# Kernel tuning notes

Measured on AMD Instinct MI355X. Metric: run time of the kernel, lower is better.

The kernel has to match this reference:

```python
import jax, jax.numpy as jnp
import numpy as np
from jax import lax

W_WIN = 7  # window size from init_kwargs


def _dwconv(x, k):
    """Depthwise 2D conv, SAME padding, kernel k: [C,1,kh,kw] (OIHW)."""
    C = x.shape[1]
    p = k.shape[-1] // 2
    return lax.conv_general_dilated(
        x, k, window_strides=(1, 1), padding=[(p, p), (p, p)],
        feature_group_count=C, dimension_numbers=("NCHW", "OIHW", "NCHW"))


def setup_inputs() -> dict:
    key = jax.random.key(0)
    ks = jax.random.split(key, 6)
    B, C, H, Wd = 1, 48, 56, 56
    x = jax.random.normal(ks[0], (B, C, H, Wd), dtype=jnp.float32)
    # small init scale keeps the softmax logits (dot/49) in a sane range
    w3 = jax.random.normal(ks[1], (C, 1, 3, 3), dtype=jnp.float32) * 0.1
    w5 = jax.random.normal(ks[2], (C, 1, 5, 5), dtype=jnp.float32) * 0.1
    w7 = jax.random.normal(ks[3], (C, 1, 7, 7), dtype=jnp.float32) * 0.1
    pw = jax.random.normal(ks[4], (C, 3 * C, 1, 1), dtype=jnp.float32) * 0.05
    pb = jax.random.normal(ks[5], (C,), dtype=jnp.float32) * 0.01
    return {"x": x, "w3": w3, "w5": w5, "w7": w7, "pw": pw, "pb": pb}


def reference(x, w3, w5, w7, pw, pb):
    B, C, H, Wd = x.shape
    w = W_WIN
    # multi-scale depthwise branch, concat on channels -> [B, 3C, H, W]
    y = jnp.concatenate([_dwconv(x, w3), _dwconv(x, w5), _dwconv(x, w7)], axis=1)
    pad_h = (-H) % w
    pad_w = (-Wd) % w
    if pad_h or pad_w:  # static Python ints -> jit-safe
        y = jnp.pad(y, ((0, 0), (0, 0), (0, pad_h), (0, pad_w)), mode="reflect")
    Hp, Wp = y.shape[2], y.shape[3]
    nH, nW = Hp // w, Wp // w
    C3 = 3 * C
    # equivalent to torch unfold(2,w,w).unfold(3,w,w).permute(0,1,2,4,3,5)
    # .reshape(B,3C,nH*nW,w*w): same row-major linearization
    yw = y.reshape(B, C3, nH * nW, w * w)
    # rows: (B, nH*nW, 3C) flattened -> N x (w*w)
    yf = yw.transpose(0, 2, 1, 3).reshape(B * nH * nW * C3, w * w)
    # full N x N self-attention over all rows (faithful to the original)
    attn = jax.nn.softmax((yf @ yf.T) / (w * w), axis=-1)
    y_hat = (attn @ yf).reshape(B, nH, nW, C3, w, w)
    y_hat = y_hat.transpose(0, 3, 1, 4, 2, 5).reshape(B, C3, nH * w, nW * w)
    y_hat = y_hat[:, :, :H, :Wd]
    # 1x1 projection 3C -> C, plus residual
    out = jnp.einsum("oi,bihw->bohw", pw[:, :, 0, 0], y_hat) + pb[None, :, None, None]
    return x + out
```

## Files before the change

kernel.cpp:

```cpp
#include <hip/hip_runtime.h>

typedef unsigned int uint;
typedef unsigned short ushort;
typedef __attribute__((ext_vector_type(8))) short bf16x8;
typedef __attribute__((ext_vector_type(4))) float f32x4;

#define C_IN   48
#define C3     144
#define HW     56
#define SSP    3136
#define DW     49
#define DPAD   64
#define NROWS  9216

#define NSPLIT 12
#define TPS    12

#define CSC 0.02944245f

#define YF_B    0
#define YFT_B   1179648
#define OPART_B 2359296
#define ESUM_B  (OPART_B + NSPLIT * DW * NROWS * 2)


__device__ __forceinline__ ushort f32_to_bf16_rne(float x) {
  uint b = __float_as_uint(x);
  b += 0x7fffu + ((b >> 16) & 1u);
  return (ushort)(b >> 16);
}
__device__ __forceinline__ float bf16_to_f32(ushort u) {
  return __uint_as_float(((uint)u) << 16);
}
__device__ __forceinline__ void async_copy16(const void* g, void* l) {
  __builtin_amdgcn_global_load_lds(
      (const __attribute__((address_space(1))) unsigned int*)g,
      (__attribute__((address_space(3))) unsigned int*)l, 16, 0, 0);
}

__global__ __launch_bounds__(256) void conv_kernel(
    const float* __restrict__ x, const float* __restrict__ w3,
    const float* __restrict__ w5, const float* __restrict__ w7,
    ushort* __restrict__ yf, ushort* __restrict__ yfT) {
  __shared__ ushort tile[4][64];
  const int tid = threadIdx.x;
  const int idx = blockIdx.x * 256 + tid;
  const int r = idx >> 6, t = idx & 63;
  const int rr = r & 3;
  const int r0 = r & ~3;

  ushort ov = 0;
  if (t < DW) {
    int g = r / C3, c3 = r - g * C3;
    int flat = g * DW + t;
    int h = flat / HW, w = flat - h * HW;
    int grp = c3 / C_IN, c = c3 - grp * C_IN;
    const float* wk; int ks;
    if (grp == 0)      { wk = w3 + c * 9;  ks = 3; }
    else if (grp == 1) { wk = w5 + c * 25; ks = 5; }
    else               { wk = w7 + c * 49; ks = 7; }
    int p = ks >> 1;
    const float* xc = x + c * SSP;
    float val = 0.f;
    for (int dy = 0; dy < ks; dy++) {
      int hy = h + dy - p;
      if (hy < 0 || hy >= HW) continue;
      const float* xr = xc + hy * HW;
      const float* wr = wk + dy * ks;
      for (int dx = 0; dx < ks; dx++) {
        int wx = w + dx - p;
        if (wx < 0 || wx >= HW) continue;
        val += xr[wx] * wr[dx];
      }
    }
    ov = f32_to_bf16_rne(val);
  }
  yf[idx] = ov;
  tile[rr][t] = ov;
  __syncthreads();

  if (tid < 64) {
    ushort4 v;
    if (tid == 56) {
      v.x = 0x3F80; v.y = 0x3F80; v.z = 0x3F80; v.w = 0x3F80;
    } else {
      v.x = tile[0][tid]; v.y = tile[1][tid];
      v.z = tile[2][tid]; v.w = tile[3][tid];
    }
    const int k6 = r0 & 63;
    const int pcol = (r0 & ~63) | (k6 & 35) | ((k6 & 12) << 1) | ((k6 & 16) >> 2);
    *(ushort4*)&yfT[tid * NROWS + pcol] = v;
  }
}

__global__ __launch_bounds__(256, 2) void attn_kernel(
    const ushort* __restrict__ yf, const ushort* __restrict__ yfT,
    ushort* __restrict__ opart, float* __restrict__ esum_g) {
  __shared__ __align__(16) char smem[32768];

  const int tid = threadIdx.x;
  const int w = tid >> 6, lane = tid & 63;
  const int q = lane >> 4, c = lane & 15;
  const int m0 = blockIdx.x * 256 + w * 64;
  const int sp = blockIdx.y;

  bf16x8 qf[4][2];
#pragma unroll
  for (int mt = 0; mt < 4; mt++)
#pragma unroll
    for (int ds = 0; ds < 2; ds++) {
      bf16x8 raw = *(const bf16x8*)&yf[(m0 + mt * 16 + c) * 64 + ds * 32 + q * 8];
      short tmp[8];
#pragma unroll
      for (int j = 0; j < 8; j++)
        tmp[j] = (short)f32_to_bf16_rne(bf16_to_f32((ushort)raw[j]) * CSC);
      qf[mt][ds] = *(bf16x8*)tmp;
    }

  f32x4 o[4][4];
#pragma unroll
  for (int dt = 0; dt < 4; dt++)
#pragma unroll
    for (int mt = 0; mt < 4; mt++) o[dt][mt] = (f32x4)0.f;

  {
    const int k0 = (sp * TPS) * 64;
    async_copy16(yf + (k0 + lane) * 64 + w * 8, smem + w * 1024);
    async_copy16(yf + (k0 + lane) * 64 + (w + 4) * 8, smem + (w + 4) * 1024);
    async_copy16(yfT + lane * NROWS + k0 + w * 8, smem + 16384 + w * 1024);
    async_copy16(yfT + lane * NROWS + k0 + (w + 4) * 8,
                 smem + 16384 + (w + 4) * 1024);
  }
  __syncthreads();

  for (int it = 0; it < TPS; it++) {
    const int cur = it & 1;
    if (it + 1 < TPS) {
      const int k1 = (sp * TPS + it + 1) * 64;
      char* Kn = smem + (cur ^ 1) * 8192;
      char* Vn = smem + 16384 + (cur ^ 1) * 8192;
      async_copy16(yf + (k1 + lane) * 64 + w * 8, Kn + w * 1024);
      async_copy16(yf + (k1 + lane) * 64 + (w + 4) * 8, Kn + (w + 4) * 1024);
      async_copy16(yfT + lane * NROWS + k1 + w * 8, Vn + w * 1024);
      async_copy16(yfT + lane * NROWS + k1 + (w + 4) * 8, Vn + (w + 4) * 1024);
    }

    const char* Kb = smem + cur * 8192;
    const char* Vb = smem + 16384 + cur * 8192;

    bf16x8 bp[4][2];
#pragma unroll
    for (int nc = 0; nc < 2; nc++) {
      f32x4 s[2][4];
#pragma unroll
      for (int h = 0; h < 2; h++) {
        const int nt = nc * 2 + h;
        bf16x8 a0 = *(const bf16x8*)(Kb + q * 1024 + (nt * 16 + c) * 16);
        bf16x8 a1 = *(const bf16x8*)(Kb + (4 + q) * 1024 + (nt * 16 + c) * 16);
#pragma unroll
        for (int mt = 0; mt < 4; mt++) {
          f32x4 acc = (f32x4)0.f;
          acc = __builtin_amdgcn_mfma_f32_16x16x32_bf16(a0, qf[mt][0], acc, 0, 0, 0);
          acc = __builtin_amdgcn_mfma_f32_16x16x32_bf16(a1, qf[mt][1], acc, 0, 0, 0);
          s[h][mt] = acc;
        }
      }
#pragma unroll
      for (int mt = 0; mt < 4; mt++) {
        uint u00 = __float_as_uint(__builtin_amdgcn_exp2f(s[0][mt][0]));
        uint u01 = __float_as_uint(__builtin_amdgcn_exp2f(s[0][mt][1]));
        uint u02 = __float_as_uint(__builtin_amdgcn_exp2f(s[0][mt][2]));
        uint u03 = __float_as_uint(__builtin_amdgcn_exp2f(s[0][mt][3]));
        uint u10 = __float_as_uint(__builtin_amdgcn_exp2f(s[1][mt][0]));
        uint u11 = __float_as_uint(__builtin_amdgcn_exp2f(s[1][mt][1]));
        uint u12 = __float_as_uint(__builtin_amdgcn_exp2f(s[1][mt][2]));
        uint u13 = __float_as_uint(__builtin_amdgcn_exp2f(s[1][mt][3]));
        uint4 t4;
        t4.x = (u00 >> 16) | (u01 & 0xffff0000u);
        t4.y = (u02 >> 16) | (u03 & 0xffff0000u);
        t4.z = (u10 >> 16) | (u11 & 0xffff0000u);
        t4.w = (u12 >> 16) | (u13 & 0xffff0000u);
        bp[mt][nc] = *(bf16x8*)&t4;
      }
    }

#pragma unroll
    for (int dt = 0; dt < 4; dt++) {
      bf16x8 v0 = *(const bf16x8*)(Vb + q * 1024 + (dt * 16 + c) * 16);
      bf16x8 v1 = *(const bf16x8*)(Vb + (4 + q) * 1024 + (dt * 16 + c) * 16);
#pragma unroll
      for (int mt = 0; mt < 4; mt++) {
        o[dt][mt] = __builtin_amdgcn_mfma_f32_16x16x32_bf16(v0, bp[mt][0], o[dt][mt], 0, 0, 0);
        o[dt][mt] = __builtin_amdgcn_mfma_f32_16x16x32_bf16(v1, bp[mt][1], o[dt][mt], 0, 0, 0);
      }
    }

    if (it + 1 < TPS) __syncthreads();
  }

#pragma unroll
  for (int dt = 0; dt < 4; dt++)
#pragma unroll
    for (int mt = 0; mt < 4; mt++)
#pragma unroll
      for (int r = 0; r < 4; r++) {
        int d = dt * 16 + q * 4 + r;
        int m = m0 + mt * 16 + c;
        float v = o[dt][mt][r];
        if (d < DW) {
          opart[(sp * DW + d) * NROWS + m] = f32_to_bf16_rne(v);
        } else if (d == 56) {
          esum_g[sp * NROWS + m] = v;
        }
      }
}

__global__ __launch_bounds__(256) void fuse_pw_kernel(
    const ushort* __restrict__ opart, const float* __restrict__ esum_g,
    const float* __restrict__ x, const float* __restrict__ pw,
    const float* __restrict__ pb, float* __restrict__ out) {
  __shared__ float vb[7 * 145];
  __shared__ float inv_es[144];
  const int g = blockIdx.x, tch = blockIdx.y;
  const int t0 = tch * 7;
  const int tid = threadIdx.x;

  if (tid < 144) {
    int r = g * C3 + tid;
    float e = 0.f;
#pragma unroll
    for (int sp = 0; sp < NSPLIT; sp++) e += esum_g[sp * NROWS + r];
    inv_es[tid] = 1.f / e;
  }
  __syncthreads();

  for (int j = tid; j < 7 * 144; j += 256) {
    int tt = j / 144, i = j - tt * 144;
    int r = g * C3 + i, t = t0 + tt;
    float ov = 0.f;
#pragma unroll
    for (int sp = 0; sp < NSPLIT; sp++)
      ov += bf16_to_f32(opart[(sp * DW + t) * NROWS + r]);
    vb[tt * 145 + i] = ov * inv_es[i];
  }
  __syncthreads();

  for (int j = tid; j < C_IN * 7; j += 256) {
    int o = j / 7, tt = j - o * 7;
    int t = t0 + tt;
    const float* pwo = pw + o * C3;
    const float* vrow = &vb[tt * 145];
    float a0 = 0.f, a1 = 0.f, a2 = 0.f, a3 = 0.f;
#pragma unroll
    for (int i = 0; i < C3; i += 4) {
      float4 wv = *(const float4*)&pwo[i];
      a0 += wv.x * vrow[i];
      a1 += wv.y * vrow[i + 1];
      a2 += wv.z * vrow[i + 2];
      a3 += wv.w * vrow[i + 3];
    }
    float acc = (a0 + a1) + (a2 + a3);
    int nh = g >> 3, nw = g & 7;
    int th = t / 7, tw = t - th * 7;
    int oidx = o * SSP + (nh * 7 + th) * HW + (nw * 7 + tw);
    out[oidx] = x[oidx] + pb[o] + acc;
  }
}

extern "C" void kernel_launch(void* const* d_in, const int* in_sizes, int n_in,
                              void* d_out, int out_size, void* d_ws, size_t ws_size,
                              hipStream_t stream) {
  const float* x  = (const float*)d_in[0];
  const float* w3 = (const float*)d_in[1];
  const float* w5 = (const float*)d_in[2];
  const float* w7 = (const float*)d_in[3];
  const float* pw = (const float*)d_in[4];
  const float* pb = (const float*)d_in[5];
  float* out = (float*)d_out;
  char* ws = (char*)d_ws;

  ushort* yf    = (ushort*)(ws + YF_B);
  ushort* yfT   = (ushort*)(ws + YFT_B);
  ushort* opart = (ushort*)(ws + OPART_B);
  float*  esum  = (float*)(ws + ESUM_B);

  conv_kernel<<<(NROWS * DPAD) / 256, 256, 0, stream>>>(x, w3, w5, w7, yf, yfT);
  attn_kernel<<<dim3(NROWS / 256, NSPLIT), 256, 0, stream>>>(yf, yfT, opart, esum);
  fuse_pw_kernel<<<dim3(64, 7), 256, 0, stream>>>(opart, esum, x, pw, pb, out);
}
```

Measured before the change: 114.6 us.

## Interleave QK and PV MFMAs per half-tile, raise attn occupancy, vectorize reduce loads

The attention inner loop now computes scores for one 32-key half, immediately exponentiates and packs them, then issues the PV MFMAs for that half. This drops the s[2][4] and bp[4][2] register arrays and should let launch bounds ask for 3 blocks per CU instead of 2. The final reduction kernel reads the split partials with 8-wide bf16 vector loads instead of scalar loads. The risks are register spills from the tighter occupancy target and less MFMA overlap within each wave.

```diff
diff --git a/kernel.cpp b/kernel.cpp
--- a/kernel.cpp
+++ b/kernel.cpp
@@ -4,6 +4,7 @@
 typedef unsigned short ushort;
 typedef __attribute__((ext_vector_type(8))) short bf16x8;
 typedef __attribute__((ext_vector_type(4))) float f32x4;
+typedef __attribute__((ext_vector_type(8))) unsigned short ushort8v;
 
 #define C_IN   48
 #define C3     144
@@ -36,6 +37,9 @@
   __builtin_amdgcn_global_load_lds(
       (const __attribute__((address_space(1))) unsigned int*)g,
       (__attribute__((address_space(3))) unsigned int*)l, 16, 0, 0);
+}
+__device__ __forceinline__ uint pack_bf16x2(float a, float b) {
+  return (__float_as_uint(a) >> 16) | (__float_as_uint(b) & 0xffff0000u);
 }
 
 __global__ __launch_bounds__(256) void conv_kernel(
@@ -93,7 +97,7 @@
   }
 }
 
-__global__ __launch_bounds__(256, 2) void attn_kernel(
+__global__ __launch_bounds__(256, 3) void attn_kernel(
     const ushort* __restrict__ yf, const ushort* __restrict__ yfT,
     ushort* __restrict__ opart, float* __restrict__ esum_g) {
   __shared__ __align__(16) char smem[32768];
@@ -148,50 +152,54 @@
     const char* Kb = smem + cur * 8192;
     const char* Vb = smem + 16384 + cur * 8192;
 
-    bf16x8 bp[4][2];
 #pragma unroll
     for (int nc = 0; nc < 2; nc++) {
-      f32x4 s[2][4];
-#pragma unroll
-      for (int h = 0; h < 2; h++) {
-        const int nt = nc * 2 + h;
-        bf16x8 a0 = *(const bf16x8*)(Kb + q * 1024 + (nt * 16 + c) * 16);
-        bf16x8 a1 = *(const bf16x8*)(Kb + (4 + q) * 1024 + (nt * 16 + c) * 16);
+      uint lo0[4], lo1[4];
+      {
+        const int row = ((nc * 2) * 16 + c) * 16;
+        bf16x8 a0 = *(const bf16x8*)(Kb + q * 1024 + row);
+        bf16x8 a1 = *(const bf16x8*)(Kb + (4 + q) * 1024 + row);
 #pragma unroll
         for (int mt = 0; mt < 4; mt++) {
           f32x4 acc = (f32x4)0.f;
           acc = __builtin_amdgcn_mfma_f32_16x16x32_bf16(a0, qf[mt][0], acc, 0, 0, 0);
           acc = __builtin_amdgcn_mfma_f32_16x16x32_bf16(a1, qf[mt][1], acc, 0, 0, 0);
-          s[h][mt] = acc;
+          float e0 = __builtin_amdgcn_exp2f(acc[0]);
+          float e1 = __builtin_amdgcn_exp2f(acc[1]);
+          float e2 = __builtin_amdgcn_exp2f(acc[2]);
+          float e3 = __builtin_amdgcn_exp2f(acc[3]);
+          lo0[mt] = pack_bf16x2(e0, e1);
+          lo1[mt] = pack_bf16x2(e2, e3);
         }
       }
-#pragma unroll
-      for (int mt = 0; mt < 4; mt++) {
-        uint u00 = __float_as_uint(__builtin_amdgcn_exp2f(s[0][mt][0]));
-        uint u01 = __float_as_uint(__builtin_amdgcn_exp2f(s[0][mt][1]));
-        uint u02 = __float_as_uint(__builtin_amdgcn_exp2f(s[0][mt][2]));
-        uint u03 = __float_as_uint(__builtin_amdgcn_exp2f(s[0][mt][3]));
-        uint u10 = __float_as_uint(__builtin_amdgcn_exp2f(s[1][mt][0]));
-        uint u11 = __float_as_uint(__builtin_amdgcn_exp2f(s[1][mt][1]));
-        uint u12 = __float_as_uint(__builtin_amdgcn_exp2f(s[1][mt][2]));
-        uint u13 = __float_as_uint(__builtin_amdgcn_exp2f(s[1][mt][3]));
-        uint4 t4;
-        t4.x = (u00 >> 16) | (u01 & 0xffff0000u);
-        t4.y = (u02 >> 16) | (u03 & 0xffff0000u);
-        t4.z = (u10 >> 16) | (u11 & 0xffff0000u);
-        t4.w = (u12 >> 16) | (u13 & 0xffff0000u);
-        bp[mt][nc] = *(bf16x8*)&t4;
-      }
-    }
-
-#pragma unroll
-    for (int dt = 0; dt < 4; dt++) {
-      bf16x8 v0 = *(const bf16x8*)(Vb + q * 1024 + (dt * 16 + c) * 16);
-      bf16x8 v1 = *(const bf16x8*)(Vb + (4 + q) * 1024 + (dt * 16 + c) * 16);
-#pragma unroll
-      for (int mt = 0; mt < 4; mt++) {
-        o[dt][mt] = __builtin_amdgcn_mfma_f32_16x16x32_bf16(v0, bp[mt][0], o[dt][mt], 0, 0, 0);
-        o[dt][mt] = __builtin_amdgcn_mfma_f32_16x16x32_bf16(v1, bp[mt][1], o[dt][mt], 0, 0, 0);
+      bf16x8 bpn[4];
+      {
+        const int row = ((nc * 2 + 1) * 16 + c) * 16;
+        bf16x8 a0 = *(const bf16x8*)(Kb + q * 1024 + row);
+        bf16x8 a1 = *(const bf16x8*)(Kb + (4 + q) * 1024 + row);
+#pragma unroll
+        for (int mt = 0; mt < 4; mt++) {
+          f32x4 acc = (f32x4)0.f;
+          acc = __builtin_amdgcn_mfma_f32_16x16x32_bf16(a0, qf[mt][0], acc, 0, 0, 0);
+          acc = __builtin_amdgcn_mfma_f32_16x16x32_bf16(a1, qf[mt][1], acc, 0, 0, 0);
+          float e0 = __builtin_amdgcn_exp2f(acc[0]);
+          float e1 = __builtin_amdgcn_exp2f(acc[1]);
+          float e2 = __builtin_amdgcn_exp2f(acc[2]);
+          float e3 = __builtin_amdgcn_exp2f(acc[3]);
+          uint4 t4;
+          t4.x = lo0[mt];
+          t4.y = lo1[mt];
+          t4.z = pack_bf16x2(e0, e1);
+          t4.w = pack_bf16x2(e2, e3);
+          bpn[mt] = *(bf16x8*)&t4;
+        }
+      }
+#pragma unroll
+      for (int dt = 0; dt < 4; dt++) {
+        bf16x8 vf = *(const bf16x8*)(Vb + (4 * nc + q) * 1024 + (dt * 16 + c) * 16);
+#pragma unroll
+        for (int mt = 0; mt < 4; mt++)
+          o[dt][mt] = __builtin_amdgcn_mfma_f32_16x16x32_bf16(vf, bpn[mt], o[dt][mt], 0, 0, 0);
       }
     }
 
@@ -234,14 +242,22 @@
   }
   __syncthreads();
 
-  for (int j = tid; j < 7 * 144; j += 256) {
-    int tt = j / 144, i = j - tt * 144;
-    int r = g * C3 + i, t = t0 + tt;
-    float ov = 0.f;
-#pragma unroll
-    for (int sp = 0; sp < NSPLIT; sp++)
-      ov += bf16_to_f32(opart[(sp * DW + t) * NROWS + r]);
-    vb[tt * 145 + i] = ov * inv_es[i];
+  for (int j = tid; j < 7 * 18; j += 256) {
+    int tt = j / 18, ch = j - tt * 18;
+    int i0 = ch * 8;
+    int t = t0 + tt;
+    float acc[8];
+#pragma unroll
+    for (int k = 0; k < 8; k++) acc[k] = 0.f;
+#pragma unroll
+    for (int sp = 0; sp < NSPLIT; sp++) {
+      ushort8v v = *(const ushort8v*)&opart[(sp * DW + t) * NROWS + g * C3 + i0];
+#pragma unroll
+      for (int k = 0; k < 8; k++) acc[k] += bf16_to_f32(v[k]);
+    }
+#pragma unroll
+    for (int k = 0; k < 8; k++)
+      vb[tt * 145 + i0 + k] = acc[k] * inv_es[i0 + k];
   }
   __syncthreads();
 
```

Measured after the change: 112.4 us. No clear change (-1.9%).
